# Optimization experiments

Measured on AMD Instinct MI355X. Metric: run time of the kernel, lower is better.

The kernel has to match this reference:

```python
import jax, jax.numpy as jnp
import numpy as np

B, T, EMB = 2, 2048, 1024
H, D = 16, 64          # n_heads, head_dim; H*D == EMB
FF = 4 * EMB


def _ln(x, w, b, eps=1e-5):
    mu = jnp.mean(x, axis=-1, keepdims=True)
    var = jnp.var(x, axis=-1, keepdims=True)
    return (x - mu) * jax.lax.rsqrt(var + eps) * w + b


def setup_inputs() -> dict:
    key = jax.random.key(0)
    ks = jax.random.split(key, 5)
    s = 0.02
    return {
        "x": jax.random.normal(ks[0], (B, T, EMB), jnp.float32),
        "ln1_w": jnp.ones((EMB,), jnp.float32),
        "ln1_b": jnp.zeros((EMB,), jnp.float32),
        "c_proj_w": jax.random.normal(ks[1], (3 * H * D, EMB), jnp.float32) * s,  # Linear(emb, 3HD, bias=False)
        "proj_w": jax.random.normal(ks[2], (EMB, H * D), jnp.float32) * s,
        "proj_b": jnp.zeros((EMB,), jnp.float32),
        "ln2_w": jnp.ones((EMB,), jnp.float32),
        "ln2_b": jnp.zeros((EMB,), jnp.float32),
        "ffn1_w": jax.random.normal(ks[3], (FF, EMB), jnp.float32) * s,
        "ffn1_b": jnp.zeros((FF,), jnp.float32),
        "ffn2_w": jax.random.normal(ks[4], (EMB, FF), jnp.float32) * s,
        "ffn2_b": jnp.zeros((EMB,), jnp.float32),
    }


def reference(x, ln1_w, ln1_b, c_proj_w, proj_w, proj_b, ln2_w, ln2_b,
              ffn1_w, ffn1_b, ffn2_w, ffn2_b):
    Bx, Tx, C = x.shape
    ln_x = _ln(x, ln1_w, ln1_b)
    c = ln_x @ c_proj_w.T                     # (B,T,3HD)
    c = c.reshape(Bx, Tx, H, 3 * D)
    k, q, v = jnp.split(c, 3, axis=-1)        # split order k,q,v as in source
    q = q.transpose(0, 2, 1, 3)               # (B,H,T,D)
    k = k.transpose(0, 2, 1, 3)
    v = v.transpose(0, 2, 1, 3)
    wei = jnp.einsum('bhqd,bhkd->bhqk', q, k) * (D ** -0.5)  # (B,H,T,T)
    mask = jnp.tril(jnp.ones((Tx, Tx), bool))
    wei = jnp.where(mask, wei, -jnp.inf)
    wei = jax.nn.softmax(wei, axis=-1)
    act = jnp.einsum('bhqk,bhkd->bhqd', wei, v)
    act = act.transpose(0, 2, 1, 3).reshape(Bx, Tx, H * D)
    act = act @ proj_w.T + proj_b
    act = x + act                              # residual 1
    h = _ln(act, ln2_w, ln2_b)
    h = jax.nn.relu(h @ ffn1_w.T + ffn1_b) @ ffn2_w.T + ffn2_b
    return x + h                               # NOTE: source adds x, not act
```

## Files before the change

kernel.cpp:

```cpp
#include <hip/hip_runtime.h>
#include <math.h>

typedef unsigned short u16;
typedef unsigned int u32;
typedef __attribute__((ext_vector_type(8))) __bf16 bf16x8;
typedef __attribute__((ext_vector_type(4))) float f32x4;

#define DEVI __device__ __forceinline__

DEVI u16 f2bf(float f){
  u32 b = __builtin_bit_cast(u32, f);
  return (u16)((b + 0x7FFFu + ((b >> 16) & 1u)) >> 16);
}

DEVI f32x4 mfma16(bf16x8 a, bf16x8 b, f32x4 c){
  return __builtin_amdgcn_mfma_f32_16x16x32_bf16(a, b, c, 0, 0, 0);
}

DEVI void gload16(const u16* g, u16* l){
  __builtin_amdgcn_global_load_lds(
      (const __attribute__((address_space(1))) u32*)g,
      (__attribute__((address_space(3))) u32*)l,
      16, 0, 0);
}

DEVI void phase_bar(){
  __builtin_amdgcn_sched_barrier(0);
  __builtin_amdgcn_s_barrier();
  __builtin_amdgcn_sched_barrier(0);
}

DEVI bf16x8 scale_bf16x8(bf16x8 v, float s){
  u32 w[4]; __builtin_memcpy(w, &v, 16);
  u32 o[4];
  #pragma unroll
  for (int i = 0; i < 4; ++i){
    float f0 = __builtin_bit_cast(float, (w[i] & 0xFFFFu) << 16) * s;
    float f1 = __builtin_bit_cast(float, w[i] & 0xFFFF0000u) * s;
    o[i] = (u32)f2bf(f0) | ((u32)f2bf(f1) << 16);
  }
  bf16x8 r; __builtin_memcpy(&r, o, 16);
  return r;
}

__global__ __launch_bounds__(256) void cvt_kernel(const float* __restrict__ in,
                                                  u16* __restrict__ out, int n4){
  int i = blockIdx.x * 256 + threadIdx.x;
  if (i >= n4) return;
  float4 v = reinterpret_cast<const float4*>(in)[i];
  u32 lo = (u32)f2bf(v.x) | ((u32)f2bf(v.y) << 16);
  u32 hi = (u32)f2bf(v.z) | ((u32)f2bf(v.w) << 16);
  reinterpret_cast<uint2*>(out)[i] = make_uint2(lo, hi);
}

__global__ __launch_bounds__(256) void ln_kernel(const float* __restrict__ x,
                                                 const float* __restrict__ w,
                                                 const float* __restrict__ b,
                                                 u16* __restrict__ out){
  int row = blockIdx.x;
  int tid = threadIdx.x;
  const float4 v = reinterpret_cast<const float4*>(x + (size_t)row * 1024)[tid];
  float s  = v.x + v.y + v.z + v.w;
  float ss = v.x*v.x + v.y*v.y + v.z*v.z + v.w*v.w;
  #pragma unroll
  for (int m = 1; m < 64; m <<= 1){
    s  += __shfl_xor(s,  m, 64);
    ss += __shfl_xor(ss, m, 64);
  }
  __shared__ float red[8];
  int wid = tid >> 6, lane = tid & 63;
  if (lane == 0){ red[wid] = s; red[4 + wid] = ss; }
  __syncthreads();
  s  = red[0] + red[1] + red[2] + red[3];
  ss = red[4] + red[5] + red[6] + red[7];
  float mu   = s * (1.0f/1024.0f);
  float var  = ss * (1.0f/1024.0f) - mu*mu;
  float rstd = rsqrtf(var + 1e-5f);
  const float4 wv = reinterpret_cast<const float4*>(w)[tid];
  const float4 bv = reinterpret_cast<const float4*>(b)[tid];
  u32 lo = (u32)f2bf((v.x-mu)*rstd*wv.x + bv.x) | ((u32)f2bf((v.y-mu)*rstd*wv.y + bv.y) << 16);
  u32 hi = (u32)f2bf((v.z-mu)*rstd*wv.z + bv.z) | ((u32)f2bf((v.w-mu)*rstd*wv.w + bv.w) << 16);
  reinterpret_cast<uint2*>(out + (size_t)row*1024)[tid] = make_uint2(lo, hi);
}

__global__ __launch_bounds__(256) void reduce4_kernel(const u16* __restrict__ P,
                                                      const float* __restrict__ x,
                                                      const float* __restrict__ bias,
                                                      float* __restrict__ out){
  const size_t i8 = ((size_t)blockIdx.x * 256 + threadIdx.x) * 8;
  const size_t PS = (size_t)4096 * 1024;
  const int col0 = (int)(i8 & 1023);
  float acc[8];
  #pragma unroll
  for (int j = 0; j < 8; ++j) acc[j] = bias[col0 + j];
  #pragma unroll
  for (int s = 0; s < 4; ++s){
    uint4 d = *reinterpret_cast<const uint4*>(P + s*PS + i8);
    u32 w[4] = {d.x, d.y, d.z, d.w};
    #pragma unroll
    for (int j = 0; j < 8; ++j){
      u32 bits = ((w[j>>1] >> (16*(j&1))) & 0xFFFFu) << 16;
      acc[j] += __builtin_bit_cast(float, bits);
    }
  }
  float4 xv0 = reinterpret_cast<const float4*>(x + i8)[0];
  float4 xv1 = reinterpret_cast<const float4*>(x + i8)[1];
  acc[0]+=xv0.x; acc[1]+=xv0.y; acc[2]+=xv0.z; acc[3]+=xv0.w;
  acc[4]+=xv1.x; acc[5]+=xv1.y; acc[6]+=xv1.z; acc[7]+=xv1.w;
  reinterpret_cast<float4*>(out + i8)[0] = make_float4(acc[0],acc[1],acc[2],acc[3]);
  reinterpret_cast<float4*>(out + i8)[1] = make_float4(acc[4],acc[5],acc[6],acc[7]);
}

template<bool HAS_BIAS, bool RELU, bool SPLIT>
__global__ __launch_bounds__(512, 2) void gemm256(const u16* __restrict__ A,
                                                  const u16* __restrict__ W,
                                                  const float* __restrict__ bias,
                                                  u16* __restrict__ outp,
                                                  int M, int N, int lda, int kLen){
  const int tid = threadIdx.x;
  const int wid = tid >> 6, lane = tid & 63;
  const int l16 = lane & 15, lhi = lane >> 4;
  const int wr = wid >> 2, wc = wid & 3;

  const int gx = gridDim.x, gy = gridDim.y;
  const int nwg = gx * gy * gridDim.z;
  const int bid = (blockIdx.z * gy + blockIdx.y) * gx + blockIdx.x;
  const int swz = (bid & 7) * (nwg >> 3) + (bid >> 3);
  const int col = swz % gx;
  const int rs  = swz / gx;
  const int row = rs % gy;
  const int ksp = rs / gy;
  const int brow = row * 256;
  const int bcol = col * 256;
  const size_t koff = (size_t)ksp * kLen;
  if (SPLIT) outp += (size_t)ksp * M * N;

  __shared__ u16 LDS[2][2][2][256*32];

  const int srow = tid >> 2;
  const int cg   = (tid & 3) ^ ((tid >> 3) & 3);
  const u16* gA = A + (size_t)(brow + srow) * lda + koff + cg*8;
  const u16* gW = W + (size_t)(bcol + srow) * lda + koff + cg*8;
  const size_t rK = (size_t)128 * lda;

#define STAGE(buf, mat, ks, t) do {                                   \
    const u16* _s = ((mat) ? gW : gA) + (t)*64 + (ks)*32;             \
    u16* _d = &LDS[buf][mat][ks][(wid*16)*32];                        \
    gload16(_s,      _d);                                             \
    gload16(_s + rK, _d + 128*32);                                    \
  } while(0)

  const int cswz = (lhi ^ ((l16 >> 1) & 3)) * 8;
  const int aoff = (wr*128 + l16)*32 + cswz;
  const int boff = (wc*64  + l16)*32 + cswz;
#define RDA(buf, ks, m) (*reinterpret_cast<const bf16x8*>(&LDS[buf][0][ks][aoff + (m)*512]))
#define RDB(buf, ks, n) (*reinterpret_cast<const bf16x8*>(&LDS[buf][1][ks][boff + (n)*512]))

  f32x4 acc[8][4] = {};
  bf16x8 a[8], b0, b1;

#define MFMA_PH(n0, n1) do {                                          \
    __builtin_amdgcn_s_setprio(1);                                    \
    _Pragma("unroll")                                                 \
    for (int m = 0; m < 8; ++m){                                      \
      acc[m][n0] = mfma16(a[m], b0, acc[m][n0]);                      \
      acc[m][n1] = mfma16(a[m], b1, acc[m][n1]);                      \
    }                                                                 \
    __builtin_amdgcn_s_setprio(0);                                    \
  } while(0)

  const int NITER = kLen >> 7;

  STAGE(0,0,0,0); STAGE(0,1,0,0); STAGE(0,0,1,0); STAGE(0,1,1,0);
  STAGE(1,0,0,1); STAGE(1,1,0,1);
  asm volatile("s_waitcnt vmcnt(4)" ::: "memory");
  phase_bar();

  for (int j = 0; j < NITER; ++j){
    const int t0 = 2*j, t1 = 2*j + 1;
    const bool more = (j + 1 < NITER);

    #pragma unroll
    for (int m = 0; m < 8; ++m) a[m] = RDA(0,0,m);
    b0 = RDB(0,0,0); b1 = RDB(0,0,1);
    STAGE(1,0,1,t1);
    phase_bar();
    MFMA_PH(0,1);
    phase_bar();
    b0 = RDB(0,0,2); b1 = RDB(0,0,3);
    STAGE(1,1,1,t1);
    phase_bar();
    MFMA_PH(2,3);
    phase_bar();
    #pragma unroll
    for (int m = 0; m < 8; ++m) a[m] = RDA(0,1,m);
    b0 = RDB(0,1,0); b1 = RDB(0,1,1);
    if (more) STAGE(0,0,0,t0+2);
    phase_bar();
    MFMA_PH(0,1);
    phase_bar();
    b0 = RDB(0,1,2); b1 = RDB(0,1,3);
    if (more){ STAGE(0,1,0,t0+2); asm volatile("s_waitcnt vmcnt(4)" ::: "memory"); }
    else     {                    asm volatile("s_waitcnt vmcnt(0)" ::: "memory"); }
    phase_bar();
    MFMA_PH(2,3);
    phase_bar();
    #pragma unroll
    for (int m = 0; m < 8; ++m) a[m] = RDA(1,0,m);
    b0 = RDB(1,0,0); b1 = RDB(1,0,1);
    if (more) STAGE(0,0,1,t0+2);
    phase_bar();
    MFMA_PH(0,1);
    phase_bar();
    b0 = RDB(1,0,2); b1 = RDB(1,0,3);
    if (more) STAGE(0,1,1,t0+2);
    phase_bar();
    MFMA_PH(2,3);
    phase_bar();
    #pragma unroll
    for (int m = 0; m < 8; ++m) a[m] = RDA(1,1,m);
    b0 = RDB(1,1,0); b1 = RDB(1,1,1);
    if (more) STAGE(1,0,0,t1+2);
    phase_bar();
    MFMA_PH(0,1);
    phase_bar();
    b0 = RDB(1,1,2); b1 = RDB(1,1,3);
    if (more){ STAGE(1,1,0,t1+2); asm volatile("s_waitcnt vmcnt(4)" ::: "memory"); }
    phase_bar();
    MFMA_PH(2,3);
    phase_bar();
  }
  __builtin_amdgcn_sched_barrier(0);

  const int row0 = brow + wr*128;
  const int col0 = bcol + wc*64;
  #pragma unroll
  for (int m = 0; m < 8; ++m){
    #pragma unroll
    for (int n = 0; n < 4; ++n){
      #pragma unroll
      for (int r = 0; r < 4; ++r){
        int row_ = row0 + m*16 + 4*lhi + r;
        int col_ = col0 + n*16 + l16;
        float v = acc[m][n][r];
        if constexpr (HAS_BIAS) v += bias[col_];
        if constexpr (RELU)     v = fmaxf(v, 0.0f);
        outp[(size_t)row_ * N + col_] = f2bf(v);
      }
    }
  }
#undef STAGE
#undef RDA
#undef RDB
#undef MFMA_PH
}

template<bool HAS_BIAS, bool HAS_RES, bool RELU, bool OUT_BF16>
__global__ __launch_bounds__(256) void gemm_bt(const u16* __restrict__ A,
                                               const u16* __restrict__ W,
                                               const float* __restrict__ bias,
                                               const float* __restrict__ res,
                                               void* __restrict__ outp,
                                               int M, int N, int K){
  const int tid = threadIdx.x;
  const int wid = tid >> 6, lane = tid & 63;
  const int l16 = lane & 15, lhi = lane >> 4;
  const int wr = wid >> 1, wc = wid & 1;

  const int gx = gridDim.x;
  const int nwg = gx * gridDim.y;
  const int bid = blockIdx.y * gx + blockIdx.x;
  const int swz = (bid & 7) * (nwg >> 3) + (bid >> 3);
  const int brow = (swz / gx) * 128;
  const int bcol = (swz % gx) * 128;

  __shared__ u16 As[2][128*32];
  __shared__ u16 Bs[2][128*32];

  const int srow = wid*32 + (lane >> 2);
  const int schk = lane & 3;
  const u16* gA0 = A + (size_t)(brow + srow)      * K + schk*8;
  const u16* gA1 = A + (size_t)(brow + srow + 16) * K + schk*8;
  const u16* gW0 = W + (size_t)(bcol + srow)      * K + schk*8;
  const u16* gW1 = W + (size_t)(bcol + srow + 16) * K + schk*8;
  const int ldsA0 = (wid*32)*32, ldsA1 = (wid*32 + 16)*32;

  f32x4 acc[4][4] = {};

  gload16(gA0, &As[0][ldsA0]);
  gload16(gA1, &As[0][ldsA1]);
  gload16(gW0, &Bs[0][ldsA0]);
  gload16(gW1, &Bs[0][ldsA1]);

  int cur = 0;
  for (int k0 = 0; k0 < K; k0 += 32){
    __syncthreads();
    if (k0 + 32 < K){
      gload16(gA0 + k0 + 32, &As[cur^1][ldsA0]);
      gload16(gA1 + k0 + 32, &As[cur^1][ldsA1]);
      gload16(gW0 + k0 + 32, &Bs[cur^1][ldsA0]);
      gload16(gW1 + k0 + 32, &Bs[cur^1][ldsA1]);
    }
    bf16x8 af[4], bfr[4];
    #pragma unroll
    for (int m = 0; m < 4; ++m)
      af[m]  = *reinterpret_cast<const bf16x8*>(&As[cur][(wr*64 + m*16 + l16)*32 + 8*lhi]);
    #pragma unroll
    for (int n = 0; n < 4; ++n)
      bfr[n] = *reinterpret_cast<const bf16x8*>(&Bs[cur][(wc*64 + n*16 + l16)*32 + 8*lhi]);
    #pragma unroll
    for (int m = 0; m < 4; ++m){
      #pragma unroll
      for (int n = 0; n < 4; ++n){
        acc[m][n] = mfma16(af[m], bfr[n], acc[m][n]);
      }
    }
    cur ^= 1;
  }

  const int row0 = brow + wr*64;
  const int col0 = bcol + wc*64;
  #pragma unroll
  for (int m = 0; m < 4; ++m){
    #pragma unroll
    for (int n = 0; n < 4; ++n){
      #pragma unroll
      for (int r = 0; r < 4; ++r){
        int row = row0 + m*16 + 4*lhi + r;
        int col = col0 + n*16 + l16;
        float v = acc[m][n][r];
        if constexpr (HAS_BIAS) v += bias[col];
        if constexpr (RELU)     v = fmaxf(v, 0.0f);
        if constexpr (HAS_RES)  v += res[(size_t)row * N + col];
        if constexpr (OUT_BF16) ((u16*)outp)[(size_t)row * N + col] = f2bf(v);
        else                    ((float*)outp)[(size_t)row * N + col] = v;
      }
    }
  }
}

__global__ __launch_bounds__(256) void attn_kernel(const u16* __restrict__ qkv,
                                                   u16* __restrict__ att){
  const int bh = blockIdx.x;
  const int qt = 31 - blockIdx.y;
  const int bb = bh >> 4, hh = bh & 15;
  const int tid = threadIdx.x;
  const int wid = tid >> 6, lane = tid & 63;
  const int l16 = lane & 15, lhi = lane >> 4;
  const u16* base = qkv + (size_t)bb * 2048 * 3072 + (size_t)hh * 192;

  __shared__ u16 Ks[64*72];
  __shared__ u16 Vt[64*80];
  __shared__ u16 Ps[4*16*80];

  const int sr = tid >> 2;
  const int sc = tid & 3;
  const u16* kstage = base + (size_t)sr * 3072 + sc*8;
  const int va = tid >> 3;
  const int vb = tid & 7;
  const u16* vstage = base + (size_t)(2*va) * 3072 + 128 + vb*8;
  const int vch = ((va >> 2) ^ vb) * 8 + 2*(va & 3);

  const int qrow0 = qt * 64 + wid * 16;

  const float QSCALE = 0.125f * 1.44269504f;
  bf16x8 qf[2];
  {
    const u16* qp = base + (size_t)(qrow0 + l16) * 3072 + 64 + 8*lhi;
    qf[0] = scale_bf16x8(*reinterpret_cast<const bf16x8*>(qp), QSCALE);
    qf[1] = scale_bf16x8(*reinterpret_cast<const bf16x8*>(qp + 32), QSCALE);
  }

  f32x4 o[4] = {};
  float m_r[4], l_part[4];
  #pragma unroll
  for (int r = 0; r < 4; ++r){ m_r[r] = -INFINITY; l_part[r] = 0.0f; }

  const int nkt = qt + 1;

  uint4 kd0, kd1, vd0, vd1;
  kd0 = *reinterpret_cast<const uint4*>(kstage);
  kd1 = *reinterpret_cast<const uint4*>(kstage + 32);
  vd0 = *reinterpret_cast<const uint4*>(vstage);
  vd1 = *reinterpret_cast<const uint4*>(vstage + 3072);

  for (int kt = 0; kt < nkt; ++kt){
    __syncthreads();
    *reinterpret_cast<uint4*>(&Ks[sr*72 + sc*8])      = kd0;
    *reinterpret_cast<uint4*>(&Ks[sr*72 + sc*8 + 32]) = kd1;
    {
      u32 w0[4] = {vd0.x, vd0.y, vd0.z, vd0.w};
      u32 w1[4] = {vd1.x, vd1.y, vd1.z, vd1.w};
      #pragma unroll
      for (int jj = 0; jj < 8; ++jj){
        u32 e0 = (w0[jj>>1] >> (16*(jj&1))) & 0xFFFFu;
        u32 e1 = (w1[jj>>1] >> (16*(jj&1))) & 0xFFFFu;
        int d = vb*8 + jj;
        *reinterpret_cast<u32*>(&Vt[d*80 + vch]) = e0 | (e1 << 16);
      }
    }
    __syncthreads();

    if (kt + 1 < nkt){
      const u16* kp = kstage + (size_t)(kt + 1) * 64 * 3072;
      const u16* vp = vstage + (size_t)(kt + 1) * 64 * 3072;
      kd0 = *reinterpret_cast<const uint4*>(kp);
      kd1 = *reinterpret_cast<const uint4*>(kp + 32);
      vd0 = *reinterpret_cast<const uint4*>(vp);
      vd1 = *reinterpret_cast<const uint4*>(vp + 3072);
    }

    const int kb = kt * 64;

    f32x4 s_acc[4] = {};
    __builtin_amdgcn_s_setprio(1);
    #pragma unroll
    for (int f = 0; f < 4; ++f){
      const u16* kp = &Ks[(f*16 + l16)*72 + 8*lhi];
      bf16x8 k0 = *reinterpret_cast<const bf16x8*>(kp);
      bf16x8 k1 = *reinterpret_cast<const bf16x8*>(kp + 32);
      s_acc[f] = mfma16(qf[0], k0, s_acc[f]);
      s_acc[f] = mfma16(qf[1], k1, s_acc[f]);
    }
    __builtin_amdgcn_s_setprio(0);

    float sc_[4][4];
    #pragma unroll
    for (int f = 0; f < 4; ++f){
      #pragma unroll
      for (int r = 0; r < 4; ++r) sc_[f][r] = s_acc[f][r];
    }

    if (kt == nkt - 1){
      #pragma unroll
      for (int f = 0; f < 4; ++f){
        int col = kb + f*16 + l16;
        #pragma unroll
        for (int r = 0; r < 4; ++r){
          int row = qrow0 + 4*lhi + r;
          if (col > row) sc_[f][r] = -INFINITY;
        }
      }
    }

    float mxl[4];
    bool need = false;
    #pragma unroll
    for (int r = 0; r < 4; ++r){
      mxl[r] = fmaxf(fmaxf(sc_[0][r], sc_[1][r]), fmaxf(sc_[2][r], sc_[3][r]));
      need |= (mxl[r] > m_r[r]);
    }
    if (__any(need)){
      #pragma unroll
      for (int r = 0; r < 4; ++r){
        float mx = mxl[r];
        #pragma unroll
        for (int m = 1; m < 16; m <<= 1) mx = fmaxf(mx, __shfl_xor(mx, m, 64));
        float mnew = fmaxf(m_r[r], mx);
        float al = exp2f(m_r[r] - mnew);
        m_r[r] = mnew;
        l_part[r] *= al;
        #pragma unroll
        for (int n = 0; n < 4; ++n) o[n][r] *= al;
      }
    }
    float p[4][4];
    #pragma unroll
    for (int r = 0; r < 4; ++r){
      float s0 = 0.0f;
      #pragma unroll
      for (int f = 0; f < 4; ++f){ p[f][r] = exp2f(sc_[f][r] - m_r[r]); s0 += p[f][r]; }
      l_part[r] += s0;
    }

    #pragma unroll
    for (int f = 0; f < 4; ++f){
      const int kk = f*16 + l16;
      #pragma unroll
      for (int r = 0; r < 4; ++r){
        const int q = 4*lhi + r;
        Ps[wid*1280 + q*80 + (((kk>>3) ^ (q&7))*8) + (kk&7)] = f2bf(p[f][r]);
      }
    }
    bf16x8 pa[2];
    pa[0] = *reinterpret_cast<const bf16x8*>(&Ps[wid*1280 + l16*80 + (((lhi    ) ^ (l16&7))*8)]);
    pa[1] = *reinterpret_cast<const bf16x8*>(&Ps[wid*1280 + l16*80 + (((lhi + 4) ^ (l16&7))*8)]);

    __builtin_amdgcn_s_setprio(1);
    #pragma unroll
    for (int n = 0; n < 4; ++n){
      const int d = n*16 + l16;
      const int dh = d >> 3;
      #pragma unroll
      for (int s = 0; s < 2; ++s){
        bf16x8 vfr = *reinterpret_cast<const bf16x8*>(&Vt[d*80 + (((lhi + 4*s) ^ dh)*8)]);
        o[n] = mfma16(pa[s], vfr, o[n]);
      }
    }
    __builtin_amdgcn_s_setprio(0);
  }

  float inv_l[4];
  #pragma unroll
  for (int r = 0; r < 4; ++r){
    float l = l_part[r];
    #pragma unroll
    for (int m = 1; m < 16; m <<= 1) l += __shfl_xor(l, m, 64);
    inv_l[r] = 1.0f / l;
  }
  #pragma unroll
  for (int n = 0; n < 4; ++n){
    #pragma unroll
    for (int r = 0; r < 4; ++r){
      int row = qrow0 + 4*lhi + r;
      int col = hh*64 + n*16 + l16;
      att[(size_t)(bb*2048 + row) * 1024 + col] = f2bf(o[n][r] * inv_l[r]);
    }
  }
}

extern "C" void kernel_launch(void* const* d_in, const int* in_sizes, int n_in,
                              void* d_out, int out_size, void* d_ws, size_t ws_size,
                              hipStream_t stream){
  const float* x        = (const float*)d_in[0];
  const float* ln1_w    = (const float*)d_in[1];
  const float* ln1_b    = (const float*)d_in[2];
  const float* c_proj_w = (const float*)d_in[3];
  const float* proj_w   = (const float*)d_in[4];
  const float* proj_b   = (const float*)d_in[5];
  const float* ln2_w    = (const float*)d_in[6];
  const float* ln2_b    = (const float*)d_in[7];
  const float* ffn1_w   = (const float*)d_in[8];
  const float* ffn1_b   = (const float*)d_in[9];
  const float* ffn2_w   = (const float*)d_in[10];
  const float* ffn2_b   = (const float*)d_in[11];

  char* p = (char*)d_ws;
  u16* Wff1  = (u16*)p;  p += (size_t)4096*1024*2;
  u16* Wff2  = (u16*)p;  p += (size_t)1024*4096*2;
  u16* QKV   = (u16*)p;  p += (size_t)4096*3072*2;
  u16* ATT   = (u16*)p;  p += (size_t)4096*1024*2;
  u16* Wqkv  = (u16*)p;  p += (size_t)3072*1024*2;
  u16* Wproj = (u16*)p;  p += (size_t)1024*1024*2;
  u16* LNb   = (u16*)p;  p += (size_t)4096*1024*2;
  float* ACT2= (float*)p;
  u16* FFN1  = QKV;
  u16* PART  = Wqkv;

  cvt_kernel<<<3072, 256, 0, stream>>>(c_proj_w, Wqkv, 786432);
  cvt_kernel<<<1024, 256, 0, stream>>>(proj_w,  Wproj, 262144);
  cvt_kernel<<<4096, 256, 0, stream>>>(ffn1_w,  Wff1, 1048576);
  cvt_kernel<<<4096, 256, 0, stream>>>(ffn2_w,  Wff2, 1048576);

  ln_kernel<<<4096, 256, 0, stream>>>(x, ln1_w, ln1_b, LNb);
  gemm256<false,false,false><<<dim3(12,16,1), 512, 0, stream>>>(LNb, Wqkv, nullptr, QKV, 4096, 3072, 1024, 1024);
  attn_kernel<<<dim3(32,32), 256, 0, stream>>>(QKV, ATT);
  gemm_bt<true ,true ,false,false><<<dim3(8,32), 256, 0, stream>>>(ATT, Wproj, proj_b, x, ACT2, 4096, 1024, 1024);
  ln_kernel<<<4096, 256, 0, stream>>>(ACT2, ln2_w, ln2_b, LNb);
  gemm256<true ,true ,false><<<dim3(16,16,1), 512, 0, stream>>>(LNb, Wff1, ffn1_b, FFN1, 4096, 4096, 1024, 1024);
  gemm256<false,false,true ><<<dim3(4,16,4), 512, 0, stream>>>(FFN1, Wff2, nullptr, PART, 4096, 1024, 4096, 1024);
  reduce4_kernel<<<2048, 256, 0, stream>>>(PART, x, ffn2_b, (float*)d_out);
}
```

Before: 249.2 us.

## Pair causal query tiles per attention block to balance work and share K/V

```diff
diff --git a/kernel.cpp b/kernel.cpp
--- a/kernel.cpp
+++ b/kernel.cpp
@@ -11,6 +11,12 @@
 DEVI u16 f2bf(float f){
   u32 b = __builtin_bit_cast(u32, f);
   return (u16)((b + 0x7FFFu + ((b >> 16) & 1u)) >> 16);
+}
+
+DEVI u16 f2bf_hw(float f){
+  u32 r;
+  asm("v_cvt_pk_bf16_f32 %0, %1, %1" : "=v"(r) : "v"(f));
+  return (u16)r;
 }
 
 DEVI f32x4 mfma16(bf16x8 a, bf16x8 b, f32x4 c){
@@ -339,10 +345,99 @@
   }
 }
 
+
+struct AChain {
+  f32x4 o[4];
+  float m_r[4], l_p[4];
+  bf16x8 qf0, qf1;
+  int qrow0;
+};
+
+DEVI void chain_qk(f32x4 s[4], const AChain& c, const u16* Ks, int l16, int lhi){
+  __builtin_amdgcn_s_setprio(1);
+  #pragma unroll
+  for (int f = 0; f < 4; ++f){
+    const u16* kp = &Ks[(f*16 + l16)*72 + 8*lhi];
+    bf16x8 k0 = *reinterpret_cast<const bf16x8*>(kp);
+    bf16x8 k1 = *reinterpret_cast<const bf16x8*>(kp + 32);
+    s[f] = mfma16(c.qf0, k0, s[f]);
+    s[f] = mfma16(c.qf1, k1, s[f]);
+  }
+  __builtin_amdgcn_s_setprio(0);
+}
+
+DEVI void chain_mask(f32x4 s[4], int kb, int qrow0, int l16, int lhi){
+  #pragma unroll
+  for (int f = 0; f < 4; ++f){
+    int col = kb + f*16 + l16;
+    #pragma unroll
+    for (int r = 0; r < 4; ++r){
+      int row = qrow0 + 4*lhi + r;
+      if (col > row) s[f][r] = -INFINITY;
+    }
+  }
+}
+
+DEVI void chain_smpw(f32x4 s[4], AChain& c, u16* Ps, int l16, int lhi){
+  float mxl[4];
+  bool need = false;
+  #pragma unroll
+  for (int r = 0; r < 4; ++r){
+    mxl[r] = fmaxf(fmaxf(s[0][r], s[1][r]), fmaxf(s[2][r], s[3][r]));
+    need |= (mxl[r] > c.m_r[r]);
+  }
+  if (__any(need)){
+    #pragma unroll
+    for (int r = 0; r < 4; ++r){
+      float mx = mxl[r];
+      #pragma unroll
+      for (int m = 1; m < 16; m <<= 1) mx = fmaxf(mx, __shfl_xor(mx, m, 64));
+      float mnew = fmaxf(c.m_r[r], mx);
+      float al = exp2f(c.m_r[r] - mnew);
+      c.m_r[r] = mnew;
+      c.l_p[r] *= al;
+      #pragma unroll
+      for (int n = 0; n < 4; ++n) c.o[n][r] *= al;
+    }
+  }
+  #pragma unroll
+  for (int f = 0; f < 4; ++f){
+    const int kk = f*16 + l16;
+    #pragma unroll
+    for (int r = 0; r < 4; ++r){
+      const int q = 4*lhi + r;
+      float p = exp2f(s[f][r] - c.m_r[r]);
+      c.l_p[r] += p;
+      Ps[q*80 + (((kk>>3) ^ (q&7))*8) + (kk&7)] = f2bf_hw(p);
+    }
+  }
+}
+
+DEVI void chain_pr(bf16x8 pa[2], const u16* Ps, int l16, int lhi){
+  pa[0] = *reinterpret_cast<const bf16x8*>(&Ps[l16*80 + (((lhi    ) ^ (l16&7))*8)]);
+  pa[1] = *reinterpret_cast<const bf16x8*>(&Ps[l16*80 + (((lhi + 4) ^ (l16&7))*8)]);
+}
+
+DEVI void chain_pv(AChain& c, const bf16x8 pa[2], const u16* Vt, int l16, int lhi){
+  __builtin_amdgcn_s_setprio(1);
+  #pragma unroll
+  for (int n = 0; n < 4; ++n){
+    const int d = n*16 + l16;
+    const int dh = d >> 3;
+    #pragma unroll
+    for (int s = 0; s < 2; ++s){
+      bf16x8 vfr = *reinterpret_cast<const bf16x8*>(&Vt[d*80 + (((lhi + 4*s) ^ dh)*8)]);
+      c.o[n] = mfma16(pa[s], vfr, c.o[n]);
+    }
+  }
+  __builtin_amdgcn_s_setprio(0);
+}
+
 __global__ __launch_bounds__(256) void attn_kernel(const u16* __restrict__ qkv,
                                                    u16* __restrict__ att){
   const int bh = blockIdx.x;
-  const int qt = 31 - blockIdx.y;
+  const int bx = blockIdx.y;
+  const int qtA = bx, qtB = 31 - bx;
   const int bb = bh >> 4, hh = bh & 15;
   const int tid = threadIdx.x;
   const int wid = tid >> 6, lane = tid & 63;
@@ -351,7 +446,8 @@
 
   __shared__ u16 Ks[64*72];
   __shared__ u16 Vt[64*80];
-  __shared__ u16 Ps[4*16*80];
+  __shared__ u16 PsA[4*16*80];
+  __shared__ u16 PsB[4*16*80];
 
   const int sr = tid >> 2;
   const int sc = tid & 3;
@@ -361,22 +457,30 @@
   const u16* vstage = base + (size_t)(2*va) * 3072 + 128 + vb*8;
   const int vch = ((va >> 2) ^ vb) * 8 + 2*(va & 3);
 
-  const int qrow0 = qt * 64 + wid * 16;
-
   const float QSCALE = 0.125f * 1.44269504f;
-  bf16x8 qf[2];
+
+  AChain A, B;
+  A.qrow0 = qtA * 64 + wid * 16;
+  B.qrow0 = qtB * 64 + wid * 16;
   {
-    const u16* qp = base + (size_t)(qrow0 + l16) * 3072 + 64 + 8*lhi;
-    qf[0] = scale_bf16x8(*reinterpret_cast<const bf16x8*>(qp), QSCALE);
-    qf[1] = scale_bf16x8(*reinterpret_cast<const bf16x8*>(qp + 32), QSCALE);
-  }
-
-  f32x4 o[4] = {};
-  float m_r[4], l_part[4];
-  #pragma unroll
-  for (int r = 0; r < 4; ++r){ m_r[r] = -INFINITY; l_part[r] = 0.0f; }
-
-  const int nkt = qt + 1;
+    const u16* qp = base + (size_t)(A.qrow0 + l16) * 3072 + 64 + 8*lhi;
+    A.qf0 = scale_bf16x8(*reinterpret_cast<const bf16x8*>(qp), QSCALE);
+    A.qf1 = scale_bf16x8(*reinterpret_cast<const bf16x8*>(qp + 32), QSCALE);
+  }
+  {
+    const u16* qp = base + (size_t)(B.qrow0 + l16) * 3072 + 64 + 8*lhi;
+    B.qf0 = scale_bf16x8(*reinterpret_cast<const bf16x8*>(qp), QSCALE);
+    B.qf1 = scale_bf16x8(*reinterpret_cast<const bf16x8*>(qp + 32), QSCALE);
+  }
+  #pragma unroll
+  for (int r = 0; r < 4; ++r){
+    A.m_r[r] = -INFINITY; A.l_p[r] = 0.0f;
+    B.m_r[r] = -INFINITY; B.l_p[r] = 0.0f;
+    #pragma unroll
+    for (int n = 0; n < 4; ++n){ A.o[n][r] = 0.0f; B.o[n][r] = 0.0f; }
+  }
+
+  const int nkt = qtB + 1;
 
   uint4 kd0, kd1, vd0, vd1;
   kd0 = *reinterpret_cast<const uint4*>(kstage);
@@ -412,109 +516,49 @@
 
     const int kb = kt * 64;
 
-    f32x4 s_acc[4] = {};
-    __builtin_amdgcn_s_setprio(1);
-    #pragma unroll
-    for (int f = 0; f < 4; ++f){
-      const u16* kp = &Ks[(f*16 + l16)*72 + 8*lhi];
-      bf16x8 k0 = *reinterpret_cast<const bf16x8*>(kp);
-      bf16x8 k1 = *reinterpret_cast<const bf16x8*>(kp + 32);
-      s_acc[f] = mfma16(qf[0], k0, s_acc[f]);
-      s_acc[f] = mfma16(qf[1], k1, s_acc[f]);
-    }
-    __builtin_amdgcn_s_setprio(0);
-
-    float sc_[4][4];
-    #pragma unroll
-    for (int f = 0; f < 4; ++f){
-      #pragma unroll
-      for (int r = 0; r < 4; ++r) sc_[f][r] = s_acc[f][r];
-    }
-
-    if (kt == nkt - 1){
-      #pragma unroll
-      for (int f = 0; f < 4; ++f){
-        int col = kb + f*16 + l16;
-        #pragma unroll
-        for (int r = 0; r < 4; ++r){
-          int row = qrow0 + 4*lhi + r;
-          if (col > row) sc_[f][r] = -INFINITY;
-        }
-      }
-    }
-
-    float mxl[4];
-    bool need = false;
+    if (kt <= qtA){
+      f32x4 sA[4] = {}, sB[4] = {};
+      chain_qk(sA, A, Ks, l16, lhi);
+      chain_qk(sB, B, Ks, l16, lhi);
+      if (kt == qtA) chain_mask(sA, kb, A.qrow0, l16, lhi);
+      chain_smpw(sA, A, &PsA[wid*1280], l16, lhi);
+      chain_smpw(sB, B, &PsB[wid*1280], l16, lhi);
+      bf16x8 paA[2], paB[2];
+      chain_pr(paA, &PsA[wid*1280], l16, lhi);
+      chain_pr(paB, &PsB[wid*1280], l16, lhi);
+      chain_pv(A, paA, Vt, l16, lhi);
+      chain_pv(B, paB, Vt, l16, lhi);
+    } else {
+      f32x4 sB[4] = {};
+      chain_qk(sB, B, Ks, l16, lhi);
+      if (kt == qtB) chain_mask(sB, kb, B.qrow0, l16, lhi);
+      chain_smpw(sB, B, &PsB[wid*1280], l16, lhi);
+      bf16x8 paB[2];
+      chain_pr(paB, &PsB[wid*1280], l16, lhi);
+      chain_pv(B, paB, Vt, l16, lhi);
+    }
+  }
+
+  #pragma unroll
+  for (int r = 0; r < 4; ++r){
+    float la = A.l_p[r], lb = B.l_p[r];
+    #pragma unroll
+    for (int m = 1; m < 16; m <<= 1){
+      la += __shfl_xor(la, m, 64);
+      lb += __shfl_xor(lb, m, 64);
+    }
+    A.l_p[r] = 1.0f / la;
+    B.l_p[r] = 1.0f / lb;
+  }
+  #pragma unroll
+  for (int n = 0; n < 4; ++n){
     #pragma unroll
     for (int r = 0; r < 4; ++r){
-      mxl[r] = fmaxf(fmaxf(sc_[0][r], sc_[1][r]), fmaxf(sc_[2][r], sc_[3][r]));
-      need |= (mxl[r] > m_r[r]);
-    }
-    if (__any(need)){
-      #pragma unroll
-      for (int r = 0; r < 4; ++r){
-        float mx = mxl[r];
-        #pragma unroll
-        for (int m = 1; m < 16; m <<= 1) mx = fmaxf(mx, __shfl_xor(mx, m, 64));
-        float mnew = fmaxf(m_r[r], mx);
-        float al = exp2f(m_r[r] - mnew);
-        m_r[r] = mnew;
-        l_part[r] *= al;
-        #pragma unroll
-        for (int n = 0; n < 4; ++n) o[n][r] *= al;
-      }
-    }
-    float p[4][4];
-    #pragma unroll
-    for (int r = 0; r < 4; ++r){
-      float s0 = 0.0f;
-      #pragma unroll
-      for (int f = 0; f < 4; ++f){ p[f][r] = exp2f(sc_[f][r] - m_r[r]); s0 += p[f][r]; }
-      l_part[r] += s0;
-    }
-
-    #pragma unroll
-    for (int f = 0; f < 4; ++f){
-      const int kk = f*16 + l16;
-      #pragma unroll
-      for (int r = 0; r < 4; ++r){
-        const int q = 4*lhi + r;
-        Ps[wid*1280 + q*80 + (((kk>>3) ^ (q&7))*8) + (kk&7)] = f2bf(p[f][r]);
-      }
-    }
-    bf16x8 pa[2];
-    pa[0] = *reinterpret_cast<const bf16x8*>(&Ps[wid*1280 + l16*80 + (((lhi    ) ^ (l16&7))*8)]);
-    pa[1] = *reinterpret_cast<const bf16x8*>(&Ps[wid*1280 + l16*80 + (((lhi + 4) ^ (l16&7))*8)]);
-
-    __builtin_amdgcn_s_setprio(1);
-    #pragma unroll
-    for (int n = 0; n < 4; ++n){
-      const int d = n*16 + l16;
-      const int dh = d >> 3;
-      #pragma unroll
-      for (int s = 0; s < 2; ++s){
-        bf16x8 vfr = *reinterpret_cast<const bf16x8*>(&Vt[d*80 + (((lhi + 4*s) ^ dh)*8)]);
-        o[n] = mfma16(pa[s], vfr, o[n]);
-      }
-    }
-    __builtin_amdgcn_s_setprio(0);
-  }
-
-  float inv_l[4];
-  #pragma unroll
-  for (int r = 0; r < 4; ++r){
-    float l = l_part[r];
-    #pragma unroll
-    for (int m = 1; m < 16; m <<= 1) l += __shfl_xor(l, m, 64);
-    inv_l[r] = 1.0f / l;
-  }
-  #pragma unroll
-  for (int n = 0; n < 4; ++n){
-    #pragma unroll
-    for (int r = 0; r < 4; ++r){
-      int row = qrow0 + 4*lhi + r;
       int col = hh*64 + n*16 + l16;
-      att[(size_t)(bb*2048 + row) * 1024 + col] = f2bf(o[n][r] * inv_l[r]);
+      int rowA = A.qrow0 + 4*lhi + r;
+      int rowB = B.qrow0 + 4*lhi + r;
+      att[(size_t)(bb*2048 + rowA) * 1024 + col] = f2bf(A.o[n][r] * A.l_p[r]);
+      att[(size_t)(bb*2048 + rowB) * 1024 + col] = f2bf(B.o[n][r] * B.l_p[r]);
     }
   }
 }
@@ -554,7 +598,7 @@
 
   ln_kernel<<<4096, 256, 0, stream>>>(x, ln1_w, ln1_b, LNb);
   gemm256<false,false,false><<<dim3(12,16,1), 512, 0, stream>>>(LNb, Wqkv, nullptr, QKV, 4096, 3072, 1024, 1024);
-  attn_kernel<<<dim3(32,32), 256, 0, stream>>>(QKV, ATT);
+  attn_kernel<<<dim3(32,16), 256, 0, stream>>>(QKV, ATT);
   gemm_bt<true ,true ,false,false><<<dim3(8,32), 256, 0, stream>>>(ATT, Wproj, proj_b, x, ACT2, 4096, 1024, 1024);
   ln_kernel<<<4096, 256, 0, stream>>>(ACT2, ln2_w, ln2_b, LNb);
   gemm256<true ,true ,false><<<dim3(16,16,1), 512, 0, stream>>>(LNb, Wff1, ffn1_b, FFN1, 4096, 4096, 1024, 1024);
```

Measured after the change: 283.4 us. 13.7% more time.

## Rewrite attention with 32x32 MFMA, transposed scores, and register-only P exchange

Applied to the files above, without the earlier changes.

```diff
diff --git a/kernel.cpp b/kernel.cpp
--- a/kernel.cpp
+++ b/kernel.cpp
@@ -5,6 +5,7 @@
 typedef unsigned int u32;
 typedef __attribute__((ext_vector_type(8))) __bf16 bf16x8;
 typedef __attribute__((ext_vector_type(4))) float f32x4;
+typedef __attribute__((ext_vector_type(16))) float f32x16;
 
 #define DEVI __device__ __forceinline__
 
@@ -13,8 +14,17 @@
   return (u16)((b + 0x7FFFu + ((b >> 16) & 1u)) >> 16);
 }
 
+DEVI u32 cvtpk(float a, float b){
+  u32 r;
+  asm("v_cvt_pk_bf16_f32 %0, %1, %2" : "=v"(r) : "v"(a), "v"(b));
+  return r;
+}
+
 DEVI f32x4 mfma16(bf16x8 a, bf16x8 b, f32x4 c){
   return __builtin_amdgcn_mfma_f32_16x16x32_bf16(a, b, c, 0, 0, 0);
+}
+DEVI f32x16 mfma32(bf16x8 a, bf16x8 b, f32x16 c){
+  return __builtin_amdgcn_mfma_f32_32x32x16_bf16(a, b, c, 0, 0, 0);
 }
 
 DEVI void gload16(const u16* g, u16* l){
@@ -339,64 +349,69 @@
   }
 }
 
-__global__ __launch_bounds__(256) void attn_kernel(const u16* __restrict__ qkv,
+__global__ __launch_bounds__(128) void attn_kernel(const u16* __restrict__ qkv,
                                                    u16* __restrict__ att){
   const int bh = blockIdx.x;
-  const int qt = 31 - blockIdx.y;
+  const int g  = 31 - blockIdx.y;
   const int bb = bh >> 4, hh = bh & 15;
   const int tid = threadIdx.x;
   const int wid = tid >> 6, lane = tid & 63;
-  const int l16 = lane & 15, lhi = lane >> 4;
+  const int l31 = lane & 31, h = lane >> 5;
   const u16* base = qkv + (size_t)bb * 2048 * 3072 + (size_t)hh * 192;
 
   __shared__ u16 Ks[64*72];
   __shared__ u16 Vt[64*80];
-  __shared__ u16 Ps[4*16*80];
-
-  const int sr = tid >> 2;
-  const int sc = tid & 3;
-  const u16* kstage = base + (size_t)sr * 3072 + sc*8;
-  const int va = tid >> 3;
-  const int vb = tid & 7;
-  const u16* vstage = base + (size_t)(2*va) * 3072 + 128 + vb*8;
-  const int vch = ((va >> 2) ^ vb) * 8 + 2*(va & 3);
-
-  const int qrow0 = qt * 64 + wid * 16;
+
+  const int sr = tid >> 1, sh2 = (tid & 1) * 32;
+  const u16* kstage = base + (size_t)sr * 3072 + sh2;
+  const int va = tid >> 2, vd = (tid & 3) * 16;
+  const u16* vstage = base + (size_t)(2*va) * 3072 + 128 + vd;
+
+  const int qrow0 = g*64 + wid*32;
+  const int q = qrow0 + l31;
 
   const float QSCALE = 0.125f * 1.44269504f;
-  bf16x8 qf[2];
+  bf16x8 qb[4];
   {
-    const u16* qp = base + (size_t)(qrow0 + l16) * 3072 + 64 + 8*lhi;
-    qf[0] = scale_bf16x8(*reinterpret_cast<const bf16x8*>(qp), QSCALE);
-    qf[1] = scale_bf16x8(*reinterpret_cast<const bf16x8*>(qp + 32), QSCALE);
-  }
-
-  f32x4 o[4] = {};
-  float m_r[4], l_part[4];
-  #pragma unroll
-  for (int r = 0; r < 4; ++r){ m_r[r] = -INFINITY; l_part[r] = 0.0f; }
-
-  const int nkt = qt + 1;
-
-  uint4 kd0, kd1, vd0, vd1;
-  kd0 = *reinterpret_cast<const uint4*>(kstage);
-  kd1 = *reinterpret_cast<const uint4*>(kstage + 32);
-  vd0 = *reinterpret_cast<const uint4*>(vstage);
-  vd1 = *reinterpret_cast<const uint4*>(vstage + 3072);
+    const u16* qp = base + (size_t)q * 3072 + 64 + 8*h;
+    #pragma unroll
+    for (int s = 0; s < 4; ++s)
+      qb[s] = scale_bf16x8(*reinterpret_cast<const bf16x8*>(qp + 16*s), QSCALE);
+  }
+
+  f32x16 o0 = (f32x16)0.0f, o1 = (f32x16)0.0f;
+  float m = -INFINITY, l = 0.0f;
+
+  const int nkt = g + 1;
+
+  uint4 ka0, ka1, ka2, ka3, v00, v01, v10, v11;
+  ka0 = *reinterpret_cast<const uint4*>(kstage);
+  ka1 = *reinterpret_cast<const uint4*>(kstage + 8);
+  ka2 = *reinterpret_cast<const uint4*>(kstage + 16);
+  ka3 = *reinterpret_cast<const uint4*>(kstage + 24);
+  v00 = *reinterpret_cast<const uint4*>(vstage);
+  v01 = *reinterpret_cast<const uint4*>(vstage + 8);
+  v10 = *reinterpret_cast<const uint4*>(vstage + 3072);
+  v11 = *reinterpret_cast<const uint4*>(vstage + 3072 + 8);
 
   for (int kt = 0; kt < nkt; ++kt){
     __syncthreads();
-    *reinterpret_cast<uint4*>(&Ks[sr*72 + sc*8])      = kd0;
-    *reinterpret_cast<uint4*>(&Ks[sr*72 + sc*8 + 32]) = kd1;
+    *reinterpret_cast<uint4*>(&Ks[sr*72 + sh2])      = ka0;
+    *reinterpret_cast<uint4*>(&Ks[sr*72 + sh2 + 8])  = ka1;
+    *reinterpret_cast<uint4*>(&Ks[sr*72 + sh2 + 16]) = ka2;
+    *reinterpret_cast<uint4*>(&Ks[sr*72 + sh2 + 24]) = ka3;
     {
-      u32 w0[4] = {vd0.x, vd0.y, vd0.z, vd0.w};
-      u32 w1[4] = {vd1.x, vd1.y, vd1.z, vd1.w};
+      u32 w00[4] = {v00.x, v00.y, v00.z, v00.w};
+      u32 w01[4] = {v01.x, v01.y, v01.z, v01.w};
+      u32 w10[4] = {v10.x, v10.y, v10.z, v10.w};
+      u32 w11[4] = {v11.x, v11.y, v11.z, v11.w};
       #pragma unroll
-      for (int jj = 0; jj < 8; ++jj){
-        u32 e0 = (w0[jj>>1] >> (16*(jj&1))) & 0xFFFFu;
-        u32 e1 = (w1[jj>>1] >> (16*(jj&1))) & 0xFFFFu;
-        int d = vb*8 + jj;
-        *reinterpret_cast<u32*>(&Vt[d*80 + vch]) = e0 | (e1 << 16);
+      for (int j = 0; j < 16; ++j){
+        u32 e0 = ((j < 8 ? w00[j>>1] : w01[(j-8)>>1]) >> (16*(j&1))) & 0xFFFFu;
+        u32 e1 = ((j < 8 ? w10[j>>1] : w11[(j-8)>>1]) >> (16*(j&1))) & 0xFFFFu;
+        int d = vd + j;
+        *reinterpret_cast<u32*>(&Vt[d*80 + (((va>>2) ^ (d>>3)) << 3) + 2*(va&3)]) =
+            e0 | (e1 << 16);
       }
     }
     __syncthreads();
@@ -404,118 +419,102 @@
     if (kt + 1 < nkt){
       const u16* kp = kstage + (size_t)(kt + 1) * 64 * 3072;
       const u16* vp = vstage + (size_t)(kt + 1) * 64 * 3072;
-      kd0 = *reinterpret_cast<const uint4*>(kp);
-      kd1 = *reinterpret_cast<const uint4*>(kp + 32);
-      vd0 = *reinterpret_cast<const uint4*>(vp);
-      vd1 = *reinterpret_cast<const uint4*>(vp + 3072);
-    }
-
-    const int kb = kt * 64;
-
-    f32x4 s_acc[4] = {};
+      ka0 = *reinterpret_cast<const uint4*>(kp);
+      ka1 = *reinterpret_cast<const uint4*>(kp + 8);
+      ka2 = *reinterpret_cast<const uint4*>(kp + 16);
+      ka3 = *reinterpret_cast<const uint4*>(kp + 24);
+      v00 = *reinterpret_cast<const uint4*>(vp);
+      v01 = *reinterpret_cast<const uint4*>(vp + 8);
+      v10 = *reinterpret_cast<const uint4*>(vp + 3072);
+      v11 = *reinterpret_cast<const uint4*>(vp + 3072 + 8);
+    }
+
+    f32x16 s0 = (f32x16)0.0f, s1 = (f32x16)0.0f;
     __builtin_amdgcn_s_setprio(1);
     #pragma unroll
-    for (int f = 0; f < 4; ++f){
-      const u16* kp = &Ks[(f*16 + l16)*72 + 8*lhi];
-      bf16x8 k0 = *reinterpret_cast<const bf16x8*>(kp);
-      bf16x8 k1 = *reinterpret_cast<const bf16x8*>(kp + 32);
-      s_acc[f] = mfma16(qf[0], k0, s_acc[f]);
-      s_acc[f] = mfma16(qf[1], k1, s_acc[f]);
+    for (int s = 0; s < 4; ++s){
+      bf16x8 kf0 = *reinterpret_cast<const bf16x8*>(&Ks[l31*72      + 16*s + 8*h]);
+      bf16x8 kf1 = *reinterpret_cast<const bf16x8*>(&Ks[(32+l31)*72 + 16*s + 8*h]);
+      s0 = mfma32(kf0, qb[s], s0);
+      s1 = mfma32(kf1, qb[s], s1);
     }
     __builtin_amdgcn_s_setprio(0);
-
-    float sc_[4][4];
-    #pragma unroll
-    for (int f = 0; f < 4; ++f){
-      #pragma unroll
-      for (int r = 0; r < 4; ++r) sc_[f][r] = s_acc[f][r];
-    }
 
     if (kt == nkt - 1){
       #pragma unroll
-      for (int f = 0; f < 4; ++f){
-        int col = kb + f*16 + l16;
-        #pragma unroll
-        for (int r = 0; r < 4; ++r){
-          int row = qrow0 + 4*lhi + r;
-          if (col > row) sc_[f][r] = -INFINITY;
-        }
+      for (int r = 0; r < 16; ++r){
+        int krow = kt*64 + (r&3) + 8*(r>>2) + 4*h;
+        if (krow > q)      s0[r] = -INFINITY;
+        if (krow + 32 > q) s1[r] = -INFINITY;
       }
     }
 
-    float mxl[4];
-    bool need = false;
-    #pragma unroll
-    for (int r = 0; r < 4; ++r){
-      mxl[r] = fmaxf(fmaxf(sc_[0][r], sc_[1][r]), fmaxf(sc_[2][r], sc_[3][r]));
-      need |= (mxl[r] > m_r[r]);
-    }
-    if (__any(need)){
-      #pragma unroll
-      for (int r = 0; r < 4; ++r){
-        float mx = mxl[r];
-        #pragma unroll
-        for (int m = 1; m < 16; m <<= 1) mx = fmaxf(mx, __shfl_xor(mx, m, 64));
-        float mnew = fmaxf(m_r[r], mx);
-        float al = exp2f(m_r[r] - mnew);
-        m_r[r] = mnew;
-        l_part[r] *= al;
-        #pragma unroll
-        for (int n = 0; n < 4; ++n) o[n][r] *= al;
-      }
-    }
-    float p[4][4];
-    #pragma unroll
-    for (int r = 0; r < 4; ++r){
-      float s0 = 0.0f;
-      #pragma unroll
-      for (int f = 0; f < 4; ++f){ p[f][r] = exp2f(sc_[f][r] - m_r[r]); s0 += p[f][r]; }
-      l_part[r] += s0;
-    }
-
-    #pragma unroll
-    for (int f = 0; f < 4; ++f){
-      const int kk = f*16 + l16;
-      #pragma unroll
-      for (int r = 0; r < 4; ++r){
-        const int q = 4*lhi + r;
-        Ps[wid*1280 + q*80 + (((kk>>3) ^ (q&7))*8) + (kk&7)] = f2bf(p[f][r]);
-      }
-    }
-    bf16x8 pa[2];
-    pa[0] = *reinterpret_cast<const bf16x8*>(&Ps[wid*1280 + l16*80 + (((lhi    ) ^ (l16&7))*8)]);
-    pa[1] = *reinterpret_cast<const bf16x8*>(&Ps[wid*1280 + l16*80 + (((lhi + 4) ^ (l16&7))*8)]);
+    float mx = s0[0];
+    #pragma unroll
+    for (int r = 1; r < 16; ++r) mx = fmaxf(mx, s0[r]);
+    #pragma unroll
+    for (int r = 0; r < 16; ++r) mx = fmaxf(mx, s1[r]);
+    mx = fmaxf(mx, __shfl_xor(mx, 32, 64));
+    if (__any(mx > m)){
+      float mnew = fmaxf(m, mx);
+      float al = exp2f(m - mnew);
+      m = mnew;
+      l *= al;
+      o0 *= al;
+      o1 *= al;
+    }
+    float p0[16], p1[16];
+    float su = 0.0f;
+    #pragma unroll
+    for (int r = 0; r < 16; ++r){ p0[r] = exp2f(s0[r] - m); su += p0[r]; }
+    #pragma unroll
+    for (int r = 0; r < 16; ++r){ p1[r] = exp2f(s1[r] - m); su += p1[r]; }
+    l += su;
+
+    u32 pk0[8], pk1[8];
+    #pragma unroll
+    for (int g4 = 0; g4 < 4; ++g4){
+      pk0[2*g4]   = cvtpk(p0[4*g4],   p0[4*g4+1]);
+      pk0[2*g4+1] = cvtpk(p0[4*g4+2], p0[4*g4+3]);
+      pk1[2*g4]   = cvtpk(p1[4*g4],   p1[4*g4+1]);
+      pk1[2*g4+1] = cvtpk(p1[4*g4+2], p1[4*g4+3]);
+    }
 
     __builtin_amdgcn_s_setprio(1);
     #pragma unroll
-    for (int n = 0; n < 4; ++n){
-      const int d = n*16 + l16;
-      const int dh = d >> 3;
-      #pragma unroll
-      for (int s = 0; s < 2; ++s){
-        bf16x8 vfr = *reinterpret_cast<const bf16x8*>(&Vt[d*80 + (((lhi + 4*s) ^ dh)*8)]);
-        o[n] = mfma16(pa[s], vfr, o[n]);
-      }
+    for (int s = 0; s < 4; ++s){
+      const int gA = (s & 1) * 2;
+      u32 oa0 = (s >> 1) ? pk1[2*gA]       : pk0[2*gA];
+      u32 oa1 = (s >> 1) ? pk1[2*gA+1]     : pk0[2*gA+1];
+      u32 ob0 = (s >> 1) ? pk1[2*(gA+1)]   : pk0[2*(gA+1)];
+      u32 ob1 = (s >> 1) ? pk1[2*(gA+1)+1] : pk0[2*(gA+1)+1];
+      u32 t0 = h ? oa0 : ob0;
+      u32 t1 = h ? oa1 : ob1;
+      u32 r0 = (u32)__shfl_xor((int)t0, 32, 64);
+      u32 r1 = (u32)__shfl_xor((int)t1, 32, 64);
+      u32 b0_ = h ? r0 : oa0;
+      u32 b1_ = h ? r1 : oa1;
+      u32 b2_ = h ? ob0 : r0;
+      u32 b3_ = h ? ob1 : r1;
+      bf16x8 pfrag = __builtin_bit_cast(bf16x8, make_uint4(b0_, b1_, b2_, b3_));
+      bf16x8 vf0 = *reinterpret_cast<const bf16x8*>(
+          &Vt[l31*80      + (((2*s + h) ^ (l31 >> 3)) << 3)]);
+      bf16x8 vf1 = *reinterpret_cast<const bf16x8*>(
+          &Vt[(32+l31)*80 + (((2*s + h) ^ ((32+l31) >> 3)) << 3)]);
+      o0 = mfma32(vf0, pfrag, o0);
+      o1 = mfma32(vf1, pfrag, o1);
     }
     __builtin_amdgcn_s_setprio(0);
   }
 
-  float inv_l[4];
-  #pragma unroll
-  for (int r = 0; r < 4; ++r){
-    float l = l_part[r];
-    #pragma unroll
-    for (int m = 1; m < 16; m <<= 1) l += __shfl_xor(l, m, 64);
-    inv_l[r] = 1.0f / l;
-  }
-  #pragma unroll
-  for (int n = 0; n < 4; ++n){
-    #pragma unroll
-    for (int r = 0; r < 4; ++r){
-      int row = qrow0 + 4*lhi + r;
-      int col = hh*64 + n*16 + l16;
-      att[(size_t)(bb*2048 + row) * 1024 + col] = f2bf(o[n][r] * inv_l[r]);
-    }
+  l += __shfl_xor(l, 32, 64);
+  float inv = 1.0f / l;
+  u16* orow = att + (size_t)(bb*2048 + q) * 1024 + hh*64;
+  #pragma unroll
+  for (int r = 0; r < 16; r += 2){
+    int d0 = (r&3) + 8*(r>>2) + 4*h;
+    *reinterpret_cast<u32*>(&orow[d0])      = cvtpk(o0[r]*inv, o0[r+1]*inv);
+    *reinterpret_cast<u32*>(&orow[32 + d0]) = cvtpk(o1[r]*inv, o1[r+1]*inv);
   }
 }
 
@@ -554,7 +553,7 @@
 
   ln_kernel<<<4096, 256, 0, stream>>>(x, ln1_w, ln1_b, LNb);
   gemm256<false,false,false><<<dim3(12,16,1), 512, 0, stream>>>(LNb, Wqkv, nullptr, QKV, 4096, 3072, 1024, 1024);
-  attn_kernel<<<dim3(32,32), 256, 0, stream>>>(QKV, ATT);
+  attn_kernel<<<dim3(32,32), 128, 0, stream>>>(QKV, ATT);
   gemm_bt<true ,true ,false,false><<<dim3(8,32), 256, 0, stream>>>(ATT, Wproj, proj_b, x, ACT2, 4096, 1024, 1024);
   ln_kernel<<<4096, 256, 0, stream>>>(ACT2, ln2_w, ln2_b, LNb);
   gemm256<true ,true ,false><<<dim3(16,16,1), 512, 0, stream>>>(LNb, Wff1, ffn1_b, FFN1, 4096, 4096, 1024, 1024);
```

Result: faster. 241.0 us (-3.3%).
